# Performance work log

Hardware: AMD Instinct MI355X
Metric: run time of the kernel (lower is better)

Reference implementation:

```python
import math
import jax
import jax.numpy as jnp
import numpy as np
from jax import lax

Q = 64          # num_quantiles (init default)
EPS = 1e-8      # eps (init default)


def setup_inputs() -> dict:
    key = jax.random.key(0)
    B, T, C = 64, 4096, 128
    x = jax.random.normal(key, (B, T, C), dtype=jnp.float32)
    return {"x": x}


def _build_quantile_table(x):
    """x: (B,T,C) -> quantiles (B,C,Q), levels (Q,). Unmasked branch."""
    B, T, C = x.shape
    levels = jnp.linspace(0.5 / Q, 1.0 - 0.5 / Q, Q, dtype=x.dtype)
    x_sorted = jnp.sort(x, axis=1)                      # (B,T,C) sorted over time
    positions = jnp.clip(levels * T - 0.5, 0.0, float(T - 1))   # (Q,)
    pos_int = jnp.clip(positions.astype(jnp.int32), 0, T - 2)   # (Q,)
    pos_frac = jnp.clip(positions - pos_int.astype(x.dtype), 0.0, 1.0)
    x_bct = jnp.transpose(x_sorted, (0, 2, 1))          # (B,C,T)
    q0 = x_bct[..., pos_int]                            # (B,C,Q)
    q1 = x_bct[..., jnp.minimum(pos_int + 1, T - 1)]    # (B,C,Q)
    quantiles = q0 * (1.0 - pos_frac) + q1 * pos_frac
    return quantiles, levels


def _interp_cdf(x_bc, q_bc, levels):
    """Piecewise-linear F_X(x): x_bc (N,T), q_bc (N,Q) monotone, levels (Q,)."""
    # batched searchsorted (right) per row
    idx = jax.vmap(lambda a, v: jnp.searchsorted(a, v, side="right"))(q_bc, x_bc)
    idx = jnp.clip(idx, 1, Q - 1)                       # (N,T)
    x0 = jnp.take_along_axis(q_bc, idx - 1, axis=-1)
    x1 = jnp.take_along_axis(q_bc, idx, axis=-1)
    y0 = levels[idx - 1]
    y1 = levels[idx]
    slope = (y1 - y0) / jnp.maximum(x1 - x0, 1e-12)
    return y0 + slope * (x_bc - x0)


def _probit(p):
    p_safe = jnp.clip(p, 1e-6, 1.0 - 1e-6)
    return jax.scipy.special.erfinv(2.0 * p_safe - 1.0) * math.sqrt(2.0)


def reference(x):
    B, T, C = x.shape
    quantiles, levels = _build_quantile_table(x)
    # torch detaches the quantile table: gradients flow through x only
    quantiles = lax.stop_gradient(quantiles)
    x_bc = jnp.transpose(x, (0, 2, 1)).reshape(B * C, T)
    q_bc = quantiles.reshape(B * C, Q)
    p_bc = jnp.clip(_interp_cdf(x_bc, q_bc, levels), EPS, 1.0 - EPS)
    z_bc = _probit(p_bc)
    return jnp.transpose(z_bc.reshape(B, C, T), (0, 2, 1))
```

## Files before the change

### kernel.cpp

```cpp
#include <hip/hip_runtime.h>
#include <math.h>

#define BB 64
#define TT 4096
#define CC 128
#define NQ 64
#define TCH2 128
#define NBKT 2048
#define NBKT_G 1024

__global__ __launch_bounds__(256) void transpose_kernel(const float* __restrict__ x,
                                                        float* __restrict__ xT) {
    __shared__ float tile[64][65];
    const int cb = blockIdx.x;
    const int tb = blockIdx.y;
    const int b  = blockIdx.z;
    const int tid = threadIdx.x;
    const int q = tid >> 6;
    const int l = tid & 63;

    const float* xs = x + ((size_t)b * TT + (size_t)tb * 64) * CC + (size_t)cb * 64;
    #pragma unroll
    for (int j = 0; j < 16; ++j) {
        int tl = q * 16 + j;
        tile[tl][l] = xs[(size_t)tl * CC + l];
    }
    __syncthreads();
    float* xd = xT + ((size_t)b * CC + (size_t)cb * 64) * TT + (size_t)tb * 64;
    #pragma unroll
    for (int j = 0; j < 16; ++j) {
        int cl = q * 16 + j;
        xd[(size_t)cl * TT + l] = tile[l][cl];
    }
}

__global__ __launch_bounds__(256) void bucket_quantile_T(const float* __restrict__ xT,
                                                         float* __restrict__ qtab) {
    __shared__ unsigned cum[NBKT];
    __shared__ unsigned cur[NBKT];
    __shared__ float    pool[TT];
    __shared__ unsigned wsum[4];

    const int row = blockIdx.x;
    const float* xrow = xT + (size_t)row * TT;
    const int tid = threadIdx.x, lane = tid & 63, wid = tid >> 6;

    float vv[16];
    #pragma unroll
    for (int j = 0; j < 4; ++j) {
        float4 v4 = ((const float4*)xrow)[j * 256 + tid];
        vv[j * 4 + 0] = v4.x; vv[j * 4 + 1] = v4.y;
        vv[j * 4 + 2] = v4.z; vv[j * 4 + 3] = v4.w;
    }

    *(uint4*)&cur[tid * 8]     = make_uint4(0u, 0u, 0u, 0u);
    *(uint4*)&cur[tid * 8 + 4] = make_uint4(0u, 0u, 0u, 0u);
    __syncthreads();

    #pragma unroll
    for (int j = 0; j < 16; ++j) {
        int bk = (int)((vv[j] + 5.0f) * 204.8f);
        bk = bk < 0 ? 0 : (bk > NBKT - 1 ? NBKT - 1 : bk);
        atomicAdd(&cur[bk], 1u);
    }
    __syncthreads();

    uint4 h0 = *(uint4*)&cur[tid * 8];
    uint4 h1 = *(uint4*)&cur[tid * 8 + 4];
    unsigned S = h0.x + h0.y + h0.z + h0.w + h1.x + h1.y + h1.z + h1.w;
    unsigned incl = S;
    #pragma unroll
    for (int off = 1; off < 64; off <<= 1) {
        unsigned n = __shfl_up(incl, off, 64);
        if (lane >= off) incl += n;
    }
    if (lane == 63) wsum[wid] = incl;
    __syncthreads();
    unsigned base = incl - S;
    for (int w = 0; w < wid; ++w) base += wsum[w];
    {
        unsigned c0 = base, c1 = c0 + h0.x, c2 = c1 + h0.y, c3 = c2 + h0.z;
        unsigned c4 = c3 + h0.w, c5 = c4 + h1.x, c6 = c5 + h1.y, c7 = c6 + h1.z;
        *(uint4*)&cum[tid * 8]     = make_uint4(c0, c1, c2, c3);
        *(uint4*)&cum[tid * 8 + 4] = make_uint4(c4, c5, c6, c7);
        *(uint4*)&cur[tid * 8]     = make_uint4(c0, c1, c2, c3);
        *(uint4*)&cur[tid * 8 + 4] = make_uint4(c4, c5, c6, c7);
    }
    __syncthreads();

    #pragma unroll
    for (int j = 0; j < 16; ++j) {
        int bk = (int)((vv[j] + 5.0f) * 204.8f);
        bk = bk < 0 ? 0 : (bk > NBKT - 1 ? NBKT - 1 : bk);
        unsigned p = atomicAdd(&cur[bk], 1u);
        pool[p] = vv[j];
    }
    __syncthreads();

    if (tid < 128) {
        const int q = tid >> 1;
        const int r = (q << 6) + 31 + (tid & 1);

        int pos = 0;
        #pragma unroll
        for (int step = 1024; step >= 1; step >>= 1) {
            int np = pos + step;
            if (np <= NBKT - 1 && (int)cum[np] <= r) pos = np;
        }
        const int segbase = (int)cum[pos];
        const int L = ((pos == NBKT - 1) ? TT : (int)cum[pos + 1]) - segbase;
        const int k = r - segbase;
        const float* seg = &pool[segbase];

        float ans = 0.0f;
        for (int i = 0; i < L; ++i) {
            float vi = seg[i];
            int rk = 0;
            for (int jj = 0; jj < L; ++jj) {
                float vj = seg[jj];
                rk += (vj < vi) || (vj == vi && jj < i);
            }
            if (rk == k) { ans = vi; break; }
        }
        float vo = __shfl_xor(ans, 1, 64);
        if ((tid & 1) == 0)
            qtab[(size_t)row * NQ + q] = (ans + vo) * 0.5f;
    }
}

__global__ __launch_bounds__(256) void bucket_quantile_G(const float* __restrict__ x,
                                                         float* __restrict__ qtab) {
    __shared__ unsigned hist[NBKT_G];
    __shared__ unsigned cum[NBKT_G];
    __shared__ unsigned cur[NBKT_G];
    __shared__ float    pool[TT];
    __shared__ unsigned wsum[4];

    const int bid = blockIdx.x;
    const int row = ((bid & 7) << 10) | (bid >> 3);
    const int b = row >> 7, c = row & (CC - 1);
    const float* xrow = x + (size_t)b * TT * CC + c;
    const int tid = threadIdx.x;
    const int lane = tid & 63, wid = tid >> 6;

    float vv[16];
    #pragma unroll
    for (int j = 0; j < 16; ++j)
        vv[j] = xrow[(size_t)((j << 8) + tid) * CC];

    *(uint4*)&hist[tid << 2] = make_uint4(0u, 0u, 0u, 0u);
    __syncthreads();

    #pragma unroll
    for (int j = 0; j < 16; ++j) {
        int bk = (int)((vv[j] + 5.0f) * 102.4f);
        bk = bk < 0 ? 0 : (bk > NBKT_G - 1 ? NBKT_G - 1 : bk);
        atomicAdd(&hist[bk], 1u);
    }
    __syncthreads();

    uint4 h = *(uint4*)&hist[tid << 2];
    unsigned S = h.x + h.y + h.z + h.w;
    unsigned incl = S;
    #pragma unroll
    for (int off = 1; off < 64; off <<= 1) {
        unsigned n = __shfl_up(incl, off, 64);
        if (lane >= off) incl += n;
    }
    if (lane == 63) wsum[wid] = incl;
    __syncthreads();
    unsigned base = incl - S;
    for (int w = 0; w < wid; ++w) base += wsum[w];
    {
        unsigned c0 = base, c1 = c0 + h.x, c2 = c1 + h.y, c3 = c2 + h.z;
        *(uint4*)&cum[tid << 2] = make_uint4(c0, c1, c2, c3);
        *(uint4*)&cur[tid << 2] = make_uint4(c0, c1, c2, c3);
    }
    __syncthreads();

    #pragma unroll
    for (int j = 0; j < 16; ++j) {
        int bk = (int)((vv[j] + 5.0f) * 102.4f);
        bk = bk < 0 ? 0 : (bk > NBKT_G - 1 ? NBKT_G - 1 : bk);
        unsigned p = atomicAdd(&cur[bk], 1u);
        pool[p] = vv[j];
    }
    __syncthreads();

    if (tid < 128) {
        const int q = tid >> 1;
        const int r = (q << 6) + 31 + (tid & 1);
        int pos = 0;
        #pragma unroll
        for (int step = 512; step >= 1; step >>= 1) {
            int np = pos + step;
            if (np <= NBKT_G - 1 && (int)cum[np] <= r) pos = np;
        }
        const int segbase = (int)cum[pos];
        const int L = (int)hist[pos];
        const int k = r - segbase;
        const float* seg = &pool[segbase];

        float ans = 0.0f;
        for (int i = 0; i < L; ++i) {
            float vi = seg[i];
            int rk = 0;
            for (int jj = 0; jj < L; ++jj) {
                float vj = seg[jj];
                rk += (vj < vi) || (vj == vi && jj < i);
            }
            if (rk == k) { ans = vi; break; }
        }
        float vo = __shfl_xor(ans, 1, 64);
        if ((tid & 1) == 0)
            qtab[(size_t)row * NQ + q] = (ans + vo) * 0.5f;
    }
}

__global__ __launch_bounds__(256) void apply_kernel(const float* __restrict__ x,
                                                    const float* __restrict__ qtab,
                                                    float* __restrict__ out) {
    __shared__ float qtT[NQ][64];
    const int b   = blockIdx.x;
    const int tch = blockIdx.y;
    const int ch  = blockIdx.z;
    const int tid = threadIdx.x;

    const float* qsrc = qtab + ((size_t)b * CC + (size_t)ch * 64) * NQ;
    for (int i = tid; i < 64 * NQ; i += 256) {
        int cl = i >> 6, k = i & 63;
        qtT[k][cl ^ k] = qsrc[i];
    }
    __syncthreads();

    const int myc = tid & 63;
    const int trow0 = tid >> 6;
    const size_t base = (size_t)b * TT * CC + (size_t)tch * TCH2 * CC
                      + (size_t)ch * 64;
    const float* xp = x + base;
    float* op = out + base;
    const float invq = 1.0f / (float)NQ;

    #pragma unroll
    for (int g = 0; g < 4; ++g) {
        float v[8];
        int   pos[8];
        int   off[8];
        #pragma unroll
        for (int e = 0; e < 8; ++e) {
            int t = trow0 + 4 * (g * 8 + e);
            off[e] = t * CC + myc;
            v[e] = xp[off[e]];
            pos[e] = 0;
        }

        #pragma unroll
        for (int step = 32; step >= 1; step >>= 1) {
            float pr[8];
            #pragma unroll
            for (int e = 0; e < 8; ++e) {
                int np = pos[e] + step - 1;
                pr[e] = qtT[np][myc ^ np];
            }
            #pragma unroll
            for (int e = 0; e < 8; ++e)
                if (pr[e] <= v[e]) pos[e] += step;
        }

        float x0[8], x1[8];
        #pragma unroll
        for (int e = 0; e < 8; ++e) {
            int idx = pos[e];
            idx = idx < 1 ? 1 : (idx > NQ - 1 ? NQ - 1 : idx);
            pos[e] = idx;
            x0[e] = qtT[idx - 1][myc ^ (idx - 1)];
            x1[e] = qtT[idx][myc ^ idx];
        }

        #pragma unroll
        for (int e = 0; e < 8; ++e) {
            const float y0 = ((float)pos[e] - 0.5f) * invq;
            const float rcp = __builtin_amdgcn_rcpf(fmaxf(x1[e] - x0[e], 1e-12f));
            float p = fmaf(invq * rcp, v[e] - x0[e], y0);
            p = fminf(fmaxf(p, 1e-6f), 1.0f - 1e-6f);

            const float xx = 2.0f * p - 1.0f;
            float w = -__logf((1.0f - xx) * (1.0f + xx));
            float z;
            if (w < 5.0f) {
                float ww = w - 2.5f;
                z = 2.81022636e-08f;
                z = fmaf(z, ww, 3.43273939e-07f);
                z = fmaf(z, ww, -3.5233877e-06f);
                z = fmaf(z, ww, -4.39150654e-06f);
                z = fmaf(z, ww, 0.00021858087f);
                z = fmaf(z, ww, -0.00125372503f);
                z = fmaf(z, ww, -0.00417768164f);
                z = fmaf(z, ww, 0.246640727f);
                z = fmaf(z, ww, 1.50140941f);
            } else {
                float ww = sqrtf(w) - 3.0f;
                z = -0.000200214257f;
                z = fmaf(z, ww, 0.000100950558f);
                z = fmaf(z, ww, 0.00134934322f);
                z = fmaf(z, ww, -0.00367342844f);
                z = fmaf(z, ww, 0.00573950773f);
                z = fmaf(z, ww, -0.0076224613f);
                z = fmaf(z, ww, 0.00943887047f);
                z = fmaf(z, ww, 1.00167406f);
                z = fmaf(z, ww, 2.83297682f);
            }
            op[off[e]] = z * xx * 1.4142135623730951f;
        }
    }
}

extern "C" void kernel_launch(void* const* d_in, const int* in_sizes, int n_in,
                              void* d_out, int out_size, void* d_ws, size_t ws_size,
                              hipStream_t stream) {
    const float* x = (const float*)d_in[0];
    float* out = (float*)d_out;
    float* qtab = (float*)d_ws;
    const size_t qtab_bytes = (size_t)BB * CC * NQ * 4;
    const size_t xT_bytes   = (size_t)BB * CC * TT * 4;

    if (ws_size >= qtab_bytes + xT_bytes) {
        float* xT = (float*)((char*)d_ws + qtab_bytes);
        dim3 tgrid(2, 64, BB);
        transpose_kernel<<<tgrid, 256, 0, stream>>>(x, xT);
        bucket_quantile_T<<<BB * CC, 256, 0, stream>>>(xT, qtab);
    } else {
        bucket_quantile_G<<<BB * CC, 256, 0, stream>>>(x, qtab);
    }
    dim3 grid(BB, TT / TCH2, 2);
    apply_kernel<<<grid, 256, 0, stream>>>(x, qtab, out);
}
```

Before: 247.2 us.

## Scatter only quantile-bearing buckets into compacted pool in bucket quantile kernel

The bucket-sort quantile kernel now flags only those histogram buckets that contain one of the 128 target ranks and compacts them into a small pool via a second scan. The scatter pass skips all other elements, which avoids most shared-memory atomics and pool writes, and each target rank's bucket is recorded directly instead of being found by binary search. The cost is an extra prefix scan, an extra barrier and more bookkeeping per thread. It also assumes 16-bit packed counts and that at most 160 buckets are flagged.

```diff
diff --git a/kernel.cpp b/kernel.cpp
--- a/kernel.cpp
+++ b/kernel.cpp
@@ -36,10 +36,13 @@
 
 __global__ __launch_bounds__(256) void bucket_quantile_T(const float* __restrict__ xT,
                                                          float* __restrict__ qtab) {
-    __shared__ unsigned cum[NBKT];
-    __shared__ unsigned cur[NBKT];
-    __shared__ float    pool[TT];
-    __shared__ unsigned wsum[4];
+    __shared__ unsigned       cum[NBKT];
+    __shared__ unsigned short flag16[NBKT];
+    __shared__ float          pool[TT];
+    __shared__ unsigned short rankinfo[128];
+    __shared__ unsigned short pb16[160];
+    __shared__ unsigned       cur2[160];
+    __shared__ unsigned       wsum[4], wsum2[4];
 
     const int row = blockIdx.x;
     const float* xrow = xT + (size_t)row * TT;
@@ -53,20 +56,21 @@
         vv[j * 4 + 2] = v4.z; vv[j * 4 + 3] = v4.w;
     }
 
-    *(uint4*)&cur[tid * 8]     = make_uint4(0u, 0u, 0u, 0u);
-    *(uint4*)&cur[tid * 8 + 4] = make_uint4(0u, 0u, 0u, 0u);
+    *(uint4*)&cum[tid * 8]     = make_uint4(0u, 0u, 0u, 0u);
+    *(uint4*)&cum[tid * 8 + 4] = make_uint4(0u, 0u, 0u, 0u);
+    *(uint4*)&flag16[tid * 8]  = make_uint4(~0u, ~0u, ~0u, ~0u);
     __syncthreads();
 
     #pragma unroll
     for (int j = 0; j < 16; ++j) {
         int bk = (int)((vv[j] + 5.0f) * 204.8f);
         bk = bk < 0 ? 0 : (bk > NBKT - 1 ? NBKT - 1 : bk);
-        atomicAdd(&cur[bk], 1u);
-    }
-    __syncthreads();
-
-    uint4 h0 = *(uint4*)&cur[tid * 8];
-    uint4 h1 = *(uint4*)&cur[tid * 8 + 4];
+        atomicAdd(&cum[bk], 1u);
+    }
+    __syncthreads();
+
+    uint4 h0 = *(uint4*)&cum[tid * 8];
+    uint4 h1 = *(uint4*)&cum[tid * 8 + 4];
     unsigned S = h0.x + h0.y + h0.z + h0.w + h1.x + h1.y + h1.z + h1.w;
     unsigned incl = S;
     #pragma unroll
@@ -78,13 +82,59 @@
     __syncthreads();
     unsigned base = incl - S;
     for (int w = 0; w < wid; ++w) base += wsum[w];
-    {
-        unsigned c0 = base, c1 = c0 + h0.x, c2 = c1 + h0.y, c3 = c2 + h0.z;
-        unsigned c4 = c3 + h0.w, c5 = c4 + h1.x, c6 = c5 + h1.y, c7 = c6 + h1.z;
-        *(uint4*)&cum[tid * 8]     = make_uint4(c0, c1, c2, c3);
-        *(uint4*)&cum[tid * 8 + 4] = make_uint4(c4, c5, c6, c7);
-        *(uint4*)&cur[tid * 8]     = make_uint4(c0, c1, c2, c3);
-        *(uint4*)&cur[tid * 8 + 4] = make_uint4(c4, c5, c6, c7);
+
+    unsigned carr[9];
+    carr[0] = base;
+    carr[1] = carr[0] + h0.x; carr[2] = carr[1] + h0.y;
+    carr[3] = carr[2] + h0.z; carr[4] = carr[3] + h0.w;
+    carr[5] = carr[4] + h1.x; carr[6] = carr[5] + h1.y;
+    carr[7] = carr[6] + h1.z; carr[8] = carr[7] + h1.w;
+    *(uint4*)&cum[tid * 8]     = make_uint4(carr[0], carr[1], carr[2], carr[3]);
+    *(uint4*)&cum[tid * 8 + 4] = make_uint4(carr[4], carr[5], carr[6], carr[7]);
+
+    unsigned flg = 0, myLen = 0, myCnt = 0;
+    #pragma unroll
+    for (int bi = 0; bi < 8; ++bi) {
+        const int cs = (int)carr[bi], ce = (int)carr[bi + 1];
+        if (ce > cs) {
+            int t0 = cs - 32;
+            int q0 = t0 < 0 ? 0 : (t0 >> 6);
+            int q1 = (ce >> 6); if (q1 > 63) q1 = 63;
+            bool any = false;
+            for (int q = q0; q <= q1; ++q) {
+                int r1 = (q << 6) + 31, r2 = r1 + 1;
+                bool i1 = (r1 >= cs) && (r1 < ce);
+                bool i2 = (r2 >= cs) && (r2 < ce);
+                if (i1) rankinfo[2 * q]     = (unsigned short)(tid * 8 + bi);
+                if (i2) rankinfo[2 * q + 1] = (unsigned short)(tid * 8 + bi);
+                any |= (i1 || i2);
+            }
+            if (any) { flg |= (1u << bi); myLen += (unsigned)(ce - cs); myCnt++; }
+        }
+    }
+
+    unsigned pk = (myLen << 16) | myCnt;
+    unsigned incl2 = pk;
+    #pragma unroll
+    for (int off = 1; off < 64; off <<= 1) {
+        unsigned n = __shfl_up(incl2, off, 64);
+        if (lane >= off) incl2 += n;
+    }
+    if (lane == 63) wsum2[wid] = incl2;
+    __syncthreads();
+    unsigned b2 = incl2 - pk;
+    for (int w = 0; w < wid; ++w) b2 += wsum2[w];
+    unsigned lenB = b2 >> 16, cntB = b2 & 0xFFFFu;
+    #pragma unroll
+    for (int bi = 0; bi < 8; ++bi) {
+        if (flg & (1u << bi)) {
+            int s = tid * 8 + bi;
+            flag16[s] = (unsigned short)cntB;
+            pb16[cntB] = (unsigned short)lenB;
+            cur2[cntB] = lenB;
+            cntB++;
+            lenB += carr[bi + 1] - carr[bi];
+        }
     }
     __syncthreads();
 
@@ -92,25 +142,23 @@
     for (int j = 0; j < 16; ++j) {
         int bk = (int)((vv[j] + 5.0f) * 204.8f);
         bk = bk < 0 ? 0 : (bk > NBKT - 1 ? NBKT - 1 : bk);
-        unsigned p = atomicAdd(&cur[bk], 1u);
-        pool[p] = vv[j];
+        unsigned short fl = flag16[bk];
+        if (fl != 0xFFFFu) {
+            unsigned p = atomicAdd(&cur2[fl], 1u);
+            pool[p] = vv[j];
+        }
     }
     __syncthreads();
 
     if (tid < 128) {
-        const int q = tid >> 1;
-        const int r = (q << 6) + 31 + (tid & 1);
-
-        int pos = 0;
-        #pragma unroll
-        for (int step = 1024; step >= 1; step >>= 1) {
-            int np = pos + step;
-            if (np <= NBKT - 1 && (int)cum[np] <= r) pos = np;
-        }
-        const int segbase = (int)cum[pos];
-        const int L = ((pos == NBKT - 1) ? TT : (int)cum[pos + 1]) - segbase;
-        const int k = r - segbase;
-        const float* seg = &pool[segbase];
+        const int j = tid;
+        const int r = ((j >> 1) << 6) + 31 + (j & 1);
+        const int s = rankinfo[j];
+        const int cs = (int)cum[s];
+        const int L = ((s < NBKT - 1) ? (int)cum[s + 1] : TT) - cs;
+        const int k = r - cs;
+        const unsigned short fid = flag16[s];
+        const float* seg = &pool[pb16[fid]];
 
         float ans = 0.0f;
         for (int i = 0; i < L; ++i) {
@@ -124,7 +172,7 @@
         }
         float vo = __shfl_xor(ans, 1, 64);
         if ((tid & 1) == 0)
-            qtab[(size_t)row * NQ + q] = (ans + vo) * 0.5f;
+            qtab[(size_t)row * NQ + (j >> 1)] = (ans + vo) * 0.5f;
     }
 }
 
```

New measurement: 247.8 us. About the same (+0.3%).
